# Optimization experiments

Hardware: AMD Instinct MI355X
Metric: run time of the kernel (lower is better)

The kernel has to match this reference:

```python
import jax, jax.numpy as jnp
import numpy as np

B, L, D, H = 2, 2048, 1024, 16
HD = D // H


def setup_inputs() -> dict:
    key = jax.random.key(0)
    ks = jax.random.split(key, 14)
    s = 0.02
    return {
        "hidden_states": jax.random.normal(ks[0], (B, L, D), jnp.float32),
        "position_embeddings": jax.random.normal(ks[1], (B, L, D), jnp.float32),
        "Wcq": jax.random.normal(ks[2], (D, D), jnp.float32) * s,
        "bcq": jnp.zeros((D,), jnp.float32),
        "Wck": jax.random.normal(ks[3], (D, D), jnp.float32) * s,
        "bck": jnp.zeros((D,), jnp.float32),
        "Wpq": jax.random.normal(ks[4], (D, D), jnp.float32) * s,
        "bpq": jnp.zeros((D,), jnp.float32),
        "Wpk": jax.random.normal(ks[5], (D, D), jnp.float32) * s,
        "bpk": jnp.zeros((D,), jnp.float32),
        "rel_bias": jnp.zeros((1, H, 1, 1), jnp.float32),
        "Wo": jax.random.normal(ks[6], (D, D), jnp.float32) * s,
        "bo": jnp.zeros((D,), jnp.float32),
    }


def _split_heads(x):
    # [B, L, D] -> [B, H, L, HD]
    b, l, _ = x.shape
    return x.reshape(b, l, H, HD).transpose(0, 2, 1, 3)


def reference(hidden_states, position_embeddings, Wcq, bcq, Wck, bck,
              Wpq, bpq, Wpk, bpk, rel_bias, Wo, bo):
    cq = _split_heads(hidden_states @ Wcq + bcq)
    ck = _split_heads(hidden_states @ Wck + bck)
    # NOTE: original code (faithfully reproduced) uses content_key as the value
    cv = ck
    pq = _split_heads(position_embeddings @ Wpq + bpq)
    pk = _split_heads(position_embeddings @ Wpk + bpk)

    scores = (jnp.einsum("bhqd,bhkd->bhqk", cq, ck)
              + jnp.einsum("bhqd,bhkd->bhqk", pq, pk)
              + rel_bias)
    attn_weights = jax.nn.softmax(scores / jnp.sqrt(jnp.float32(HD)), axis=-1)
    ctx = jnp.einsum("bhqk,bhkd->bhqd", attn_weights, cv)
    ctx = ctx.transpose(0, 2, 1, 3).reshape(hidden_states.shape[0], -1, D)
    output = ctx @ Wo + bo
    return output, attn_weights
```

## Files before the change

### kernel.cpp

```cpp
#include <hip/hip_runtime.h>
#include <hip/hip_bf16.h>
#include <math.h>


#define Bc 2
#define Lc 2048
#define Dc 1024
#define Hc 16
#define Mc (Bc*Lc)
#define NT 32

typedef __attribute__((ext_vector_type(8))) __bf16 bf16x8;
typedef __attribute__((ext_vector_type(4))) float f32x4;
typedef __attribute__((ext_vector_type(16))) float f32x16;
typedef __attribute__((ext_vector_type(2))) unsigned u32x2;

union U4 { unsigned u[4]; bf16x8 v; };

__device__ __forceinline__ void gl_lds16(const void* g, void* l) {
    __builtin_amdgcn_global_load_lds(
        (const __attribute__((address_space(1))) void*)g,
        (__attribute__((address_space(3))) void*)l, 16, 0, 0);
}
__device__ __forceinline__ unsigned pkbf(float a, float b) {
    unsigned short ua = __builtin_bit_cast(unsigned short, (__bf16)a);
    unsigned short ub = __builtin_bit_cast(unsigned short, (__bf16)b);
    return (unsigned)ua | ((unsigned)ub << 16);
}
__device__ __forceinline__ float lo2f(unsigned u){ return __builtin_bit_cast(float, u << 16); }
__device__ __forceinline__ float hi2f(unsigned u){ return __builtin_bit_cast(float, u & 0xffff0000u); }
#define E2(x) __builtin_amdgcn_exp2f(x)

#define WAIT_VM0  asm volatile("s_waitcnt vmcnt(0)" ::: "memory")
#define WAIT_VM4  asm volatile("s_waitcnt vmcnt(4)" ::: "memory")
#define WAIT_VM6  asm volatile("s_waitcnt vmcnt(6)" ::: "memory")
#define WAIT_VM8  asm volatile("s_waitcnt vmcnt(8)" ::: "memory")
#define WAIT_VM12 asm volatile("s_waitcnt vmcnt(12)" ::: "memory")
#define WAIT_LG0  asm volatile("s_waitcnt lgkmcnt(0)" ::: "memory")
#define SBAR __builtin_amdgcn_sched_barrier(0)
#define BARRIER do { __builtin_amdgcn_sched_barrier(0); __builtin_amdgcn_s_barrier(); __builtin_amdgcn_sched_barrier(0); } while (0)

__global__ __launch_bounds__(256) void prep_kernel(
    const float* __restrict__ hidden, const float* __restrict__ pos,
    const float* __restrict__ Wcq, const float* __restrict__ Wck,
    const float* __restrict__ Wpq, const float* __restrict__ Wpk,
    const float* __restrict__ Wo,
    __bf16* __restrict__ Wt, __bf16* __restrict__ Woh, __bf16* __restrict__ Wol,
    __bf16* __restrict__ Xh, __bf16* __restrict__ Xp)
{
    const int z = blockIdx.z;
    const int t = threadIdx.x;
    if (z >= 5) {
        const float* X = (z==5) ? hidden : pos;
        __bf16* dst    = (z==5) ? Xh : Xp;
        const size_t base = ((size_t)(blockIdx.y*16 + blockIdx.x)*256 + t) * 128;
        #pragma unroll
        for (int c = 0; c < 16; ++c) {
            const float* sp = X + base + c*8;
            float4 v0 = *(const float4*)sp;
            float4 v1 = *(const float4*)(sp + 4);
            bf16x8 o;
            o[0]=(__bf16)v0.x; o[1]=(__bf16)v0.y; o[2]=(__bf16)v0.z; o[3]=(__bf16)v0.w;
            o[4]=(__bf16)v1.x; o[5]=(__bf16)v1.y; o[6]=(__bf16)v1.z; o[7]=(__bf16)v1.w;
            *(bf16x8*)(dst + base + c*8) = o;
        }
        return;
    }
    const float* W = (z==0)?Wcq:(z==1)?Wck:(z==2)?Wpq:(z==3)?Wpk:Wo;
    const int n  = blockIdx.x*64 + (t & 63);
    const int k0 = blockIdx.y*128 + (t >> 6)*32;
    float v[32];
    #pragma unroll
    for (int j = 0; j < 32; ++j) v[j] = W[(size_t)(k0+j)*Dc + n];
    if (z < 4) {
        __bf16* dst = Wt + (size_t)z*Dc*Dc + (size_t)n*Dc + k0;
        #pragma unroll
        for (int c = 0; c < 4; ++c) {
            bf16x8 o;
            #pragma unroll
            for (int j = 0; j < 8; ++j) o[j] = (__bf16)v[c*8+j];
            *(bf16x8*)(dst + c*8) = o;
        }
    } else {
        __bf16* dh = Woh + (size_t)n*Dc + k0;
        __bf16* dl = Wol + (size_t)n*Dc + k0;
        #pragma unroll
        for (int c = 0; c < 4; ++c) {
            bf16x8 oh, ol;
            #pragma unroll
            for (int j = 0; j < 8; ++j) {
                float x = v[c*8+j];
                __bf16 hi = (__bf16)x;
                oh[j] = hi; ol[j] = (__bf16)(x - (float)hi);
            }
            *(bf16x8*)(dh + c*8) = oh;
            *(bf16x8*)(dl + c*8) = ol;
        }
    }
}

__global__ __launch_bounds__(256) void proj_kernel(
    const __bf16* __restrict__ Xh, const __bf16* __restrict__ Xp,
    const __bf16* __restrict__ Wt,
    const float* __restrict__ bcq, const float* __restrict__ bck,
    const float* __restrict__ bpq, const float* __restrict__ bpk,
    __bf16* __restrict__ Qc, __bf16* __restrict__ Kc)
{
    const int g = blockIdx.x;
    const int nblk = g >> 7, sg = g & 127, mblk = sg & 31, z = sg >> 5;
    const int m0 = mblk*128, n0 = nblk*128;
    const __bf16* X = (z < 2) ? Xh : Xp;
    const __bf16* Wz = Wt + (size_t)z*Dc*Dc;
    const float* bias = (z==0)?bcq:(z==1)?bck:(z==2)?bpq:bpk;
    __bf16* dst = (z & 1) ? Kc : Qc;
    const int half = z >> 1;
    const float scale = (z & 1) ? 1.0f : 0.18033688011112042f;

    const int t = threadIdx.x, lane = t & 63, w = t >> 6;
    const int wm = w >> 1, wn = w & 1;

    __shared__ __align__(16) char smem[49152];

    const int brow4 = lane >> 2;
    const int bcol  = ((lane & 3) ^ (brow4 & 3)) * 8;

    f32x4 acc[4][4] = {};

    #define STAGE_P(B, KT) do { \
        const int k0_ = (KT)*32; \
        _Pragma("unroll") \
        for (int i = 0; i < 2; ++i) { \
            int row = 16*(2*w+i) + brow4; \
            gl_lds16(X  + (size_t)(m0+row)*Dc + k0_ + bcol, smem + (B)*16384 + (2*w+i)*1024); \
            gl_lds16(Wz + (size_t)(n0+row)*Dc + k0_ + bcol, smem + (B)*16384 + 8192 + (2*w+i)*1024); \
        } \
    } while (0)

    STAGE_P(0, 0); STAGE_P(1, 1);
    WAIT_VM4; BARRIER;
    for (int kt = 0; kt < 32; ++kt) {
        if (kt+2 < 32) STAGE_P((kt+2) % 3, kt+2);
        SBAR;
        const int buf = kt % 3;
        bf16x8 a[4], b[4];
        const int s2 = lane >> 4;
        #pragma unroll
        for (int i = 0; i < 4; ++i) {
            int Ra = wm*64 + i*16 + (lane&15);
            int Rb = wn*64 + i*16 + (lane&15);
            a[i] = *(const bf16x8*)(smem + buf*16384 + Ra*64 + ((s2 ^ (Ra&3))*16));
            b[i] = *(const bf16x8*)(smem + buf*16384 + 8192 + Rb*64 + ((s2 ^ (Rb&3))*16));
        }
        __builtin_amdgcn_s_setprio(1);
        #pragma unroll
        for (int mi = 0; mi < 4; ++mi)
            #pragma unroll
            for (int ni = 0; ni < 4; ++ni)
                acc[mi][ni] = __builtin_amdgcn_mfma_f32_16x16x32_bf16(a[mi], b[ni], acc[mi][ni], 0, 0, 0);
        __builtin_amdgcn_s_setprio(0);
        if (kt+2 < 32) { WAIT_VM4; } else { WAIT_VM0; }
        BARRIER;
    }
    #undef STAGE_P
    #pragma unroll
    for (int mi = 0; mi < 4; ++mi)
        #pragma unroll
        for (int ni = 0; ni < 4; ++ni)
            #pragma unroll
            for (int r = 0; r < 4; ++r) {
                int row = m0 + wm*64 + mi*16 + (lane>>4)*4 + r;
                int col = n0 + wn*64 + ni*16 + (lane&15);
                float v = (acc[mi][ni][r] + bias[col]) * scale;
                int bb = row >> 11, l = row & (Lc-1);
                int hh = col >> 6,  hd = col & 63;
                dst[(((size_t)bb*Hc + hh)*Lc + l)*128 + half*64 + hd] = (__bf16)v;
            }
}

__global__ __launch_bounds__(256) void vt_kernel(
    const __bf16* __restrict__ Kc, __bf16* __restrict__ VT)
{
    const int l0 = blockIdx.x * 128, hb = blockIdx.y;
    const int t = threadIdx.x, w = t >> 6, lane = t & 63;
    __shared__ __bf16 T[128][72];
    const __bf16* src = Kc + ((size_t)hb*Lc + l0)*128;
    {
        const int lr = t >> 3, cc = t & 7;
        #pragma unroll
        for (int j = 0; j < 4; ++j)
            *(bf16x8*)&T[lr + j*32][cc*8] = *(const bf16x8*)(src + (size_t)(lr + j*32)*128 + cc*8);
    }
    __syncthreads();
    {
        const int d = lane;
        __bf16* dstp = VT + ((size_t)hb*64 + d)*Lc + l0 + w*32;
        #pragma unroll
        for (int j = 0; j < 4; ++j) {
            bf16x8 o;
            #pragma unroll
            for (int i = 0; i < 8; ++i) o[i] = T[w*32 + j*8 + i][d];
            *(bf16x8*)(dstp + j*8) = o;
        }
    }
}

__global__ __launch_bounds__(256, 3) void attn1_kernel(
    const __bf16* __restrict__ Qc, const __bf16* __restrict__ Kc,
    const float* __restrict__ rel_bias, float* __restrict__ baddp)
{
    const int g = blockIdx.x;
    const int qt = g >> 5, hb = g & 31, h = hb & 15;
    const int q0 = qt * 128;
    const int t = threadIdx.x, lane = t & 63, w = t >> 6;
    const int ln31 = lane & 31, hi = lane >> 5;

    const __bf16* Qp = Qc + (size_t)hb * Lc * 128;
    const __bf16* Kp = Kc + (size_t)hb * Lc * 128;

    __shared__ __align__(16) char smem[49152];

    bf16x8 qa[8];
    {
        const __bf16* qrow = Qp + (size_t)(q0 + w*32 + ln31) * 128 + hi*8;
        #pragma unroll
        for (int ks = 0; ks < 8; ++ks) qa[ks] = *(const bf16x8*)(qrow + ks*16);
    }

    int kof[4];
    #pragma unroll
    for (int c = 0; c < 4; ++c) {
        int rl = c*4 + (lane >> 4);
        int rr = w*16 + rl;
        kof[c] = rr*128 + (((lane & 15) ^ rl) * 8);
    }
    int kR[8];
    #pragma unroll
    for (int ks = 0; ks < 8; ++ks) kR[ks] = ((ks*2 + hi) ^ (lane & 15)) * 8;

    #define STAGE_K(B, KT) do { \
        const __bf16* kb_ = Kp + (size_t)(KT)*8192; \
        gl_lds16(kb_ + kof[0], smem + ((B)*64 + w*16 +  0)*256); \
        gl_lds16(kb_ + kof[1], smem + ((B)*64 + w*16 +  4)*256); \
        gl_lds16(kb_ + kof[2], smem + ((B)*64 + w*16 +  8)*256); \
        gl_lds16(kb_ + kof[3], smem + ((B)*64 + w*16 + 12)*256); \
    } while (0)
    #define KB(B, ROW, KS) (*(const bf16x8*)(smem + ((B)*64 + (ROW))*256 + kR[KS]*2))

    const float bc = rel_bias[h] * 0.18033688011112042f;
    float lp[4] = {0.f, 0.f, 0.f, 0.f};

    STAGE_K(0, 0); STAGE_K(1, 1);
    WAIT_VM4; BARRIER;
    for (int kt = 0; kt < NT; ++kt) {
        if (kt+2 < NT) STAGE_K((kt+2) % 3, kt+2);
        SBAR;
        const int buf = kt % 3;
        f32x16 s0, s1;
        #pragma unroll
        for (int r = 0; r < 16; ++r) { s0[r] = bc; s1[r] = bc; }
        __builtin_amdgcn_s_setprio(1);
        #pragma unroll
        for (int ks = 0; ks < 8; ++ks) {
            bf16x8 kb0 = KB(buf, ln31, ks);
            bf16x8 kb1 = KB(buf, 32 + ln31, ks);
            s0 = __builtin_amdgcn_mfma_f32_32x32x16_bf16(kb0, qa[ks], s0, 0, 0, 0);
            s1 = __builtin_amdgcn_mfma_f32_32x32x16_bf16(kb1, qa[ks], s1, 0, 0, 0);
        }
        __builtin_amdgcn_s_setprio(0);
        #pragma unroll
        for (int r = 0; r < 16; ++r) {
            lp[r & 3] += E2(s0[r]);
            lp[r & 3] += E2(s1[r]);
        }
        if (kt+2 < NT) { WAIT_VM4; } else { WAIT_VM0; }
        BARRIER;
    }
    float lsum = (lp[0] + lp[1]) + (lp[2] + lp[3]);
    lsum += __shfl_xor(lsum, 32);
    if (!hi) baddp[(size_t)hb*Lc + q0 + w*32 + ln31] = bc - log2f(lsum);
    #undef STAGE_K
    #undef KB
}

__global__ __launch_bounds__(256, 2) void attn2_kernel(
    const __bf16* __restrict__ Qc, const __bf16* __restrict__ Kc,
    const __bf16* __restrict__ VT, const float* __restrict__ baddp,
    float* __restrict__ attn, __bf16* __restrict__ ctxh)
{
    const int g = blockIdx.x;
    const int qt = g >> 5, hb = g & 31, h = hb & 15, bb = hb >> 4;
    const int q0 = qt * 128;
    const int t = threadIdx.x, lane = t & 63, w = t >> 6;
    const int ln31 = lane & 31, hi = lane >> 5;

    const __bf16* Qp = Qc + (size_t)hb * Lc * 128;
    const __bf16* Kp = Kc + (size_t)hb * Lc * 128;
    const __bf16* Vp = VT + (size_t)hb * 64 * Lc;

    __shared__ __align__(16) char smem[81920];
    char* const VsB = smem + 49152;
    char* const PsW = smem + 65536 + w*4096;

    bf16x8 qa[8];
    {
        const __bf16* qrow = Qp + (size_t)(q0 + w*32 + ln31) * 128 + hi*8;
        #pragma unroll
        for (int ks = 0; ks < 8; ++ks) qa[ks] = *(const bf16x8*)(qrow + ks*16);
    }
    const float badd = baddp[(size_t)hb*Lc + q0 + w*32 + ln31];

    int kof[4];
    #pragma unroll
    for (int c = 0; c < 4; ++c) {
        int rl = c*4 + (lane >> 4);
        int rr = w*16 + rl;
        kof[c] = rr*128 + (((lane & 15) ^ rl) * 8);
    }
    int vof[2];
    #pragma unroll
    for (int c = 0; c < 2; ++c) {
        int dl = lane >> 3;
        int dd = w*16 + c*8 + dl;
        vof[c] = dd*2048 + (((lane & 7) ^ dl) * 8);
    }
    int kR[8];
    #pragma unroll
    for (int ks = 0; ks < 8; ++ks) kR[ks] = ((ks*2 + hi) ^ (lane & 15)) * 8;
    int vR[4];
    #pragma unroll
    for (int ks = 0; ks < 4; ++ks) vR[ks] = ((ks*2 + hi) ^ (lane & 7)) * 8;

    #define STAGE_K(B, KT) do { \
        const __bf16* kb_ = Kp + (size_t)(KT)*8192; \
        gl_lds16(kb_ + kof[0], smem + ((B)*64 + w*16 +  0)*256); \
        gl_lds16(kb_ + kof[1], smem + ((B)*64 + w*16 +  4)*256); \
        gl_lds16(kb_ + kof[2], smem + ((B)*64 + w*16 +  8)*256); \
        gl_lds16(kb_ + kof[3], smem + ((B)*64 + w*16 + 12)*256); \
    } while (0)
    #define STAGE_V(B, KT) do { \
        const __bf16* vb_ = Vp + (KT)*64; \
        gl_lds16(vb_ + vof[0], VsB + ((B)*64 + w*16 + 0)*128); \
        gl_lds16(vb_ + vof[1], VsB + ((B)*64 + w*16 + 8)*128); \
    } while (0)
    #define KB(B, ROW, KS) (*(const bf16x8*)(smem + ((B)*64 + (ROW))*256 + kR[KS]*2))
    #define VB(B, ROW, KS) (*(const bf16x8*)(VsB  + ((B)*64 + (ROW))*128 + vR[KS]*2))

    f32x16 ctx0 = {}, ctx1 = {};
    float* abase = attn + ((size_t)hb*Lc + q0 + w*32)*Lc;
    const int rr2 = lane >> 4;
    const int s8  = lane & 15;

    STAGE_K(0, 0); STAGE_V(0, 0); STAGE_K(1, 1);
    WAIT_VM4; BARRIER;

    for (int kt = 0; kt < NT; ++kt) {
        if (kt+1 < NT) STAGE_V((kt+1) & 1, kt+1);
        if (kt+2 < NT) STAGE_K((kt+2) % 3, kt+2);
        SBAR;
        const int buf = kt % 3;
        f32x16 s0, s1;
        #pragma unroll
        for (int r = 0; r < 16; ++r) { s0[r] = badd; s1[r] = badd; }
        __builtin_amdgcn_s_setprio(1);
        #pragma unroll
        for (int ks = 0; ks < 8; ++ks) {
            bf16x8 kb0 = KB(buf, ln31, ks);
            bf16x8 kb1 = KB(buf, 32 + ln31, ks);
            s0 = __builtin_amdgcn_mfma_f32_32x32x16_bf16(kb0, qa[ks], s0, 0, 0, 0);
            s1 = __builtin_amdgcn_mfma_f32_32x32x16_bf16(kb1, qa[ks], s1, 0, 0, 0);
        }
        __builtin_amdgcn_s_setprio(0);
        unsigned u0[8], u1[8], r0[8], r1[8];
        #pragma unroll
        for (int gq = 0; gq < 4; ++gq) {
            u0[gq]   = pkbf(E2(s0[4*gq+0]), E2(s0[4*gq+1]));
            u1[gq]   = pkbf(E2(s0[4*gq+2]), E2(s0[4*gq+3]));
            u0[4+gq] = pkbf(E2(s1[4*gq+0]), E2(s1[4*gq+1]));
            u1[4+gq] = pkbf(E2(s1[4*gq+2]), E2(s1[4*gq+3]));
        }
        #pragma unroll
        for (int gq = 0; gq < 8; ++gq) {
            r0[gq] = __shfl_xor(u0[gq], 32);
            r1[gq] = __shfl_xor(u1[gq], 32);
        }
        bf16x8 pb[4];
        #pragma unroll
        for (int ks = 0; ks < 4; ++ks) {
            const int gq = 2*ks + hi;
            U4 u;
            u.u[0] = hi ? r0[gq] : u0[gq];
            u.u[1] = hi ? r1[gq] : u1[gq];
            u.u[2] = hi ? u0[gq] : r0[gq];
            u.u[3] = hi ? u1[gq] : r1[gq];
            pb[ks] = u.v;
            *(bf16x8*)(PsW + ln31*128 + ((gq ^ (ln31 & 7))*16)) = u.v;
        }
        __builtin_amdgcn_s_setprio(1);
        #pragma unroll
        for (int ks = 0; ks < 4; ++ks) {
            bf16x8 v0 = VB(kt & 1, ln31, ks);
            bf16x8 v1 = VB(kt & 1, 32 + ln31, ks);
            ctx0 = __builtin_amdgcn_mfma_f32_32x32x16_bf16(pb[ks], v0, ctx0, 0, 0, 0);
            ctx1 = __builtin_amdgcn_mfma_f32_32x32x16_bf16(pb[ks], v1, ctx1, 0, 0, 0);
        }
        __builtin_amdgcn_s_setprio(0);
        WAIT_LG0; SBAR;
        #pragma unroll
        for (int j = 0; j < 8; ++j) {
            const int row = j*4 + rr2;
            u32x2 d = *(const u32x2*)(PsW + row*128 + (((s8>>1) ^ (row&7))*16) + (s8&1)*8);
            f32x4 o;
            o[0]=lo2f(d[0]); o[1]=hi2f(d[0]); o[2]=lo2f(d[1]); o[3]=hi2f(d[1]);
            __builtin_nontemporal_store(o, (f32x4*)(abase + (size_t)row*Lc + kt*64 + s8*4));
        }
        if (kt+1 < NT) {
            if (kt+2 < NT) { WAIT_VM12; } else { WAIT_VM8; }
            BARRIER;
        }
    }

    #pragma unroll
    for (int r = 0; r < 16; ++r) {
        const int R = (r&3) + 8*(r>>2) + 4*hi;
        const size_t row = (size_t)bb*Lc + q0 + w*32 + R;
        ctxh[row*Dc + h*64 + ln31]      = (__bf16)ctx0[r];
        ctxh[row*Dc + h*64 + 32 + ln31] = (__bf16)ctx1[r];
    }
    #undef STAGE_K
    #undef STAGE_V
    #undef KB
    #undef VB
}

__global__ __launch_bounds__(256) void out_kernel(
    const __bf16* __restrict__ ctxh, const __bf16* __restrict__ Woh,
    const __bf16* __restrict__ Wol, const float* __restrict__ bo,
    float* __restrict__ out)
{
    const int m0 = blockIdx.y * 128, n0 = blockIdx.x * 128;
    const int t = threadIdx.x, lane = t & 63, w = t >> 6;
    const int wm = w >> 1, wn = w & 1;

    __shared__ __align__(16) char smem[73728];

    const int row4 = lane >> 2;
    const int scol = ((lane & 3) ^ (row4 & 3)) * 8;

    f32x4 acc[4][4] = {};

    #define STAGE_O(B, KT) do { \
        const int k0_ = (KT)*32; \
        _Pragma("unroll") \
        for (int i = 0; i < 2; ++i) { \
            int row = 16*(2*w+i) + row4; \
            gl_lds16(ctxh + (size_t)(m0+row)*Dc + k0_ + scol, smem + (B)*24576 + (2*w+i)*1024); \
            gl_lds16(Woh  + (size_t)(n0+row)*Dc + k0_ + scol, smem + (B)*24576 + 8192 + (2*w+i)*1024); \
            gl_lds16(Wol  + (size_t)(n0+row)*Dc + k0_ + scol, smem + (B)*24576 + 16384 + (2*w+i)*1024); \
        } \
    } while (0)

    STAGE_O(0, 0); STAGE_O(1, 1);
    WAIT_VM6; BARRIER;
    for (int kt = 0; kt < 32; ++kt) {
        if (kt+2 < 32) STAGE_O((kt+2) % 3, kt+2);
        SBAR;
        const int buf = kt % 3;
        bf16x8 a[4], bh[4], bl[4];
        const int s2 = lane >> 4;
        #pragma unroll
        for (int i = 0; i < 4; ++i) {
            int Ra = wm*64 + i*16 + (lane&15);
            int Rb = wn*64 + i*16 + (lane&15);
            a[i]  = *(const bf16x8*)(smem + buf*24576 + Ra*64 + ((s2 ^ (Ra&3))*16));
            bh[i] = *(const bf16x8*)(smem + buf*24576 + 8192 + Rb*64 + ((s2 ^ (Rb&3))*16));
            bl[i] = *(const bf16x8*)(smem + buf*24576 + 16384 + Rb*64 + ((s2 ^ (Rb&3))*16));
        }
        __builtin_amdgcn_s_setprio(1);
        #pragma unroll
        for (int mi = 0; mi < 4; ++mi)
            #pragma unroll
            for (int ni = 0; ni < 4; ++ni) {
                acc[mi][ni] = __builtin_amdgcn_mfma_f32_16x16x32_bf16(a[mi], bh[ni], acc[mi][ni], 0, 0, 0);
                acc[mi][ni] = __builtin_amdgcn_mfma_f32_16x16x32_bf16(a[mi], bl[ni], acc[mi][ni], 0, 0, 0);
            }
        __builtin_amdgcn_s_setprio(0);
        if (kt+2 < 32) { WAIT_VM6; } else { WAIT_VM0; }
        BARRIER;
    }
    #undef STAGE_O
    #pragma unroll
    for (int mi = 0; mi < 4; ++mi)
        #pragma unroll
        for (int ni = 0; ni < 4; ++ni)
            #pragma unroll
            for (int r = 0; r < 4; ++r) {
                int row = m0 + wm*64 + mi*16 + (lane>>4)*4 + r;
                int col = n0 + wn*64 + ni*16 + (lane&15);
                __builtin_nontemporal_store(acc[mi][ni][r] + bo[col],
                                            out + (size_t)row * Dc + col);
            }
}

extern "C" void kernel_launch(void* const* d_in, const int* in_sizes, int n_in,
                              void* d_out, int out_size, void* d_ws, size_t ws_size,
                              hipStream_t stream)
{
    const float* hidden = (const float*)d_in[0];
    const float* pos    = (const float*)d_in[1];
    const float* Wcq = (const float*)d_in[2];  const float* bcq = (const float*)d_in[3];
    const float* Wck = (const float*)d_in[4];  const float* bck = (const float*)d_in[5];
    const float* Wpq = (const float*)d_in[6];  const float* bpq = (const float*)d_in[7];
    const float* Wpk = (const float*)d_in[8];  const float* bpk = (const float*)d_in[9];
    const float* relb = (const float*)d_in[10];
    const float* Wo  = (const float*)d_in[11]; const float* bo  = (const float*)d_in[12];

    float* out  = (float*)d_out;
    float* attn = out + (size_t)Mc * Dc;

    __bf16* ws   = (__bf16*)d_ws;
    __bf16* Woh  = ws;
    __bf16* Wol  = ws + (1u<<20);
    __bf16* Wt   = ws + (2u<<20);
    __bf16* ctxh = Wt;
    __bf16* Qc   = ws + (6u<<20);
    __bf16* Kc   = ws + (14u<<20);
    __bf16* VTb  = ws + (22u<<20);
    float*  badd = (float*)(ws + (26u<<20));

    __bf16* Xh = (__bf16*)attn;
    __bf16* Xp = Xh + (4u<<20);

    prep_kernel<<<dim3(16, 8, 7), 256, 0, stream>>>(
        hidden, pos, Wcq, Wck, Wpq, Wpk, Wo, Wt, Woh, Wol, Xh, Xp);
    proj_kernel<<<dim3(1024), 256, 0, stream>>>(Xh, Xp, Wt, bcq, bck, bpq, bpk, Qc, Kc);
    vt_kernel<<<dim3(Lc/128, 32), 256, 0, stream>>>(Kc, VTb);
    attn1_kernel<<<dim3(512), 256, 0, stream>>>(Qc, Kc, relb, badd);
    attn2_kernel<<<dim3(512), 256, 0, stream>>>(Qc, Kc, VTb, badd, attn, ctxh);
    out_kernel<<<dim3(8, 32), 256, 0, stream>>>(ctxh, Woh, Wol, bo, out);
}
```

Measured before the change: 310.1 us.

## Double attention block size to 256 query rows with 8 waves sharing K/V tiles

Both attention kernels now run 512-thread blocks that each cover 256 query rows, so each staged K and V tile in LDS is shared by twice as many waves and each wave issues half as many global-to-LDS loads. The grid is halved, and the vmcnt wait counts are reduced to match the smaller per-wave load count. attn2 shared memory grows to hold per-wave P scratch for 8 waves. The cost is fewer blocks (256 on a large GPU), lower occupancy per CU, and barriers that now synchronize 8 waves.

```diff
diff --git a/kernel.cpp b/kernel.cpp
--- a/kernel.cpp
+++ b/kernel.cpp
@@ -32,10 +32,11 @@
 #define E2(x) __builtin_amdgcn_exp2f(x)
 
 #define WAIT_VM0  asm volatile("s_waitcnt vmcnt(0)" ::: "memory")
+#define WAIT_VM2  asm volatile("s_waitcnt vmcnt(2)" ::: "memory")
 #define WAIT_VM4  asm volatile("s_waitcnt vmcnt(4)" ::: "memory")
 #define WAIT_VM6  asm volatile("s_waitcnt vmcnt(6)" ::: "memory")
 #define WAIT_VM8  asm volatile("s_waitcnt vmcnt(8)" ::: "memory")
-#define WAIT_VM12 asm volatile("s_waitcnt vmcnt(12)" ::: "memory")
+#define WAIT_VM10 asm volatile("s_waitcnt vmcnt(10)" ::: "memory")
 #define WAIT_LG0  asm volatile("s_waitcnt lgkmcnt(0)" ::: "memory")
 #define SBAR __builtin_amdgcn_sched_barrier(0)
 #define BARRIER do { __builtin_amdgcn_sched_barrier(0); __builtin_amdgcn_s_barrier(); __builtin_amdgcn_sched_barrier(0); } while (0)
@@ -204,13 +205,13 @@
     }
 }
 
-__global__ __launch_bounds__(256, 3) void attn1_kernel(
+__global__ __launch_bounds__(512, 4) void attn1_kernel(
     const __bf16* __restrict__ Qc, const __bf16* __restrict__ Kc,
     const float* __restrict__ rel_bias, float* __restrict__ baddp)
 {
     const int g = blockIdx.x;
     const int qt = g >> 5, hb = g & 31, h = hb & 15;
-    const int q0 = qt * 128;
+    const int q0 = qt * 256;
     const int t = threadIdx.x, lane = t & 63, w = t >> 6;
     const int ln31 = lane & 31, hi = lane >> 5;
 
@@ -226,12 +227,11 @@
         for (int ks = 0; ks < 8; ++ks) qa[ks] = *(const bf16x8*)(qrow + ks*16);
     }
 
-    int kof[4];
-    #pragma unroll
-    for (int c = 0; c < 4; ++c) {
-        int rl = c*4 + (lane >> 4);
-        int rr = w*16 + rl;
-        kof[c] = rr*128 + (((lane & 15) ^ rl) * 8);
+    int kof[2];
+    #pragma unroll
+    for (int c = 0; c < 2; ++c) {
+        int rr = w*8 + c*4 + (lane >> 4);
+        kof[c] = rr*128 + (((lane & 15) ^ (rr & 15)) * 8);
     }
     int kR[8];
     #pragma unroll
@@ -239,18 +239,16 @@
 
     #define STAGE_K(B, KT) do { \
         const __bf16* kb_ = Kp + (size_t)(KT)*8192; \
-        gl_lds16(kb_ + kof[0], smem + ((B)*64 + w*16 +  0)*256); \
-        gl_lds16(kb_ + kof[1], smem + ((B)*64 + w*16 +  4)*256); \
-        gl_lds16(kb_ + kof[2], smem + ((B)*64 + w*16 +  8)*256); \
-        gl_lds16(kb_ + kof[3], smem + ((B)*64 + w*16 + 12)*256); \
+        gl_lds16(kb_ + kof[0], smem + (B)*16384 + (w*8 + 0)*256); \
+        gl_lds16(kb_ + kof[1], smem + (B)*16384 + (w*8 + 4)*256); \
     } while (0)
-    #define KB(B, ROW, KS) (*(const bf16x8*)(smem + ((B)*64 + (ROW))*256 + kR[KS]*2))
+    #define KB(B, ROW, KS) (*(const bf16x8*)(smem + (B)*16384 + (ROW)*256 + kR[KS]*2))
 
     const float bc = rel_bias[h] * 0.18033688011112042f;
     float lp[4] = {0.f, 0.f, 0.f, 0.f};
 
     STAGE_K(0, 0); STAGE_K(1, 1);
-    WAIT_VM4; BARRIER;
+    WAIT_VM2; BARRIER;
     for (int kt = 0; kt < NT; ++kt) {
         if (kt+2 < NT) STAGE_K((kt+2) % 3, kt+2);
         SBAR;
@@ -272,7 +270,7 @@
             lp[r & 3] += E2(s0[r]);
             lp[r & 3] += E2(s1[r]);
         }
-        if (kt+2 < NT) { WAIT_VM4; } else { WAIT_VM0; }
+        if (kt+2 < NT) { WAIT_VM2; } else { WAIT_VM0; }
         BARRIER;
     }
     float lsum = (lp[0] + lp[1]) + (lp[2] + lp[3]);
@@ -282,14 +280,14 @@
     #undef KB
 }
 
-__global__ __launch_bounds__(256, 2) void attn2_kernel(
+__global__ __launch_bounds__(512, 2) void attn2_kernel(
     const __bf16* __restrict__ Qc, const __bf16* __restrict__ Kc,
     const __bf16* __restrict__ VT, const float* __restrict__ baddp,
     float* __restrict__ attn, __bf16* __restrict__ ctxh)
 {
     const int g = blockIdx.x;
     const int qt = g >> 5, hb = g & 31, h = hb & 15, bb = hb >> 4;
-    const int q0 = qt * 128;
+    const int q0 = qt * 256;
     const int t = threadIdx.x, lane = t & 63, w = t >> 6;
     const int ln31 = lane & 31, hi = lane >> 5;
 
@@ -297,7 +295,7 @@
     const __bf16* Kp = Kc + (size_t)hb * Lc * 128;
     const __bf16* Vp = VT + (size_t)hb * 64 * Lc;
 
-    __shared__ __align__(16) char smem[81920];
+    __shared__ __align__(16) char smem[98304];
     char* const VsB = smem + 49152;
     char* const PsW = smem + 65536 + w*4096;
 
@@ -309,19 +307,17 @@
     }
     const float badd = baddp[(size_t)hb*Lc + q0 + w*32 + ln31];
 
-    int kof[4];
-    #pragma unroll
-    for (int c = 0; c < 4; ++c) {
-        int rl = c*4 + (lane >> 4);
-        int rr = w*16 + rl;
-        kof[c] = rr*128 + (((lane & 15) ^ rl) * 8);
-    }
-    int vof[2];
+    int kof[2];
     #pragma unroll
     for (int c = 0; c < 2; ++c) {
+        int rr = w*8 + c*4 + (lane >> 4);
+        kof[c] = rr*128 + (((lane & 15) ^ (rr & 15)) * 8);
+    }
+    int vof;
+    {
         int dl = lane >> 3;
-        int dd = w*16 + c*8 + dl;
-        vof[c] = dd*2048 + (((lane & 7) ^ dl) * 8);
+        int dd = w*8 + dl;
+        vof = dd*2048 + (((lane & 7) ^ dl) * 8);
     }
     int kR[8];
     #pragma unroll
@@ -332,18 +328,15 @@
 
     #define STAGE_K(B, KT) do { \
         const __bf16* kb_ = Kp + (size_t)(KT)*8192; \
-        gl_lds16(kb_ + kof[0], smem + ((B)*64 + w*16 +  0)*256); \
-        gl_lds16(kb_ + kof[1], smem + ((B)*64 + w*16 +  4)*256); \
-        gl_lds16(kb_ + kof[2], smem + ((B)*64 + w*16 +  8)*256); \
-        gl_lds16(kb_ + kof[3], smem + ((B)*64 + w*16 + 12)*256); \
+        gl_lds16(kb_ + kof[0], smem + (B)*16384 + (w*8 + 0)*256); \
+        gl_lds16(kb_ + kof[1], smem + (B)*16384 + (w*8 + 4)*256); \
     } while (0)
     #define STAGE_V(B, KT) do { \
         const __bf16* vb_ = Vp + (KT)*64; \
-        gl_lds16(vb_ + vof[0], VsB + ((B)*64 + w*16 + 0)*128); \
-        gl_lds16(vb_ + vof[1], VsB + ((B)*64 + w*16 + 8)*128); \
+        gl_lds16(vb_ + vof, VsB + (B)*8192 + (w*8)*128); \
     } while (0)
-    #define KB(B, ROW, KS) (*(const bf16x8*)(smem + ((B)*64 + (ROW))*256 + kR[KS]*2))
-    #define VB(B, ROW, KS) (*(const bf16x8*)(VsB  + ((B)*64 + (ROW))*128 + vR[KS]*2))
+    #define KB(B, ROW, KS) (*(const bf16x8*)(smem + (B)*16384 + (ROW)*256 + kR[KS]*2))
+    #define VB(B, ROW, KS) (*(const bf16x8*)(VsB  + (B)*8192 + (ROW)*128 + vR[KS]*2))
 
     f32x16 ctx0 = {}, ctx1 = {};
     float* abase = attn + ((size_t)hb*Lc + q0 + w*32)*Lc;
@@ -351,7 +344,7 @@
     const int s8  = lane & 15;
 
     STAGE_K(0, 0); STAGE_V(0, 0); STAGE_K(1, 1);
-    WAIT_VM4; BARRIER;
+    WAIT_VM2; BARRIER;
 
     for (int kt = 0; kt < NT; ++kt) {
         if (kt+1 < NT) STAGE_V((kt+1) & 1, kt+1);
@@ -414,7 +407,7 @@
             __builtin_nontemporal_store(o, (f32x4*)(abase + (size_t)row*Lc + kt*64 + s8*4));
         }
         if (kt+1 < NT) {
-            if (kt+2 < NT) { WAIT_VM12; } else { WAIT_VM8; }
+            if (kt+2 < NT) { WAIT_VM10; } else { WAIT_VM8; }
             BARRIER;
         }
     }
@@ -534,7 +527,7 @@
         hidden, pos, Wcq, Wck, Wpq, Wpk, Wo, Wt, Woh, Wol, Xh, Xp);
     proj_kernel<<<dim3(1024), 256, 0, stream>>>(Xh, Xp, Wt, bcq, bck, bpq, bpk, Qc, Kc);
     vt_kernel<<<dim3(Lc/128, 32), 256, 0, stream>>>(Kc, VTb);
-    attn1_kernel<<<dim3(512), 256, 0, stream>>>(Qc, Kc, relb, badd);
-    attn2_kernel<<<dim3(512), 256, 0, stream>>>(Qc, Kc, VTb, badd, attn, ctxh);
+    attn1_kernel<<<dim3(256), 512, 0, stream>>>(Qc, Kc, relb, badd);
+    attn2_kernel<<<dim3(256), 512, 0, stream>>>(Qc, Kc, VTb, badd, attn, ctxh);
     out_kernel<<<dim3(8, 32), 256, 0, stream>>>(ctxh, Woh, Wol, bo, out);
 }
```

Result: faster. 282.3 us (-9.0%).
